# Kernel optimization log

Hardware: AMD Instinct MI355X
Metric: run time of the kernel (lower is better)

The kernel has to match this reference:

```python
import jax, jax.numpy as jnp
import numpy as np

D = 128        # feature_dims
ITERS = 2      # update_iters
B, R = 8, 256  # n segments (proteins), residues per segment
NEG_SLOPE = 0.1

def leaky(x):
    return jax.nn.leaky_relu(x, NEG_SLOPE)

def setup_inputs() -> dict:
    key = jax.random.key(0)
    ks = jax.random.split(key, 13)
    def w(k, shape):
        fan_in = shape[0]
        return jax.random.normal(k, shape, jnp.float32) / np.sqrt(fan_in)
    return {
        "fresidues": jax.random.normal(ks[0], (B, R, 20), jnp.float32),
        "coordinates": jax.random.normal(ks[1], (B, R, 3), jnp.float32) * 10.0,
        "W_emb": w(ks[2], (20, D)),                    # res_embedding (no bias)
        "W_e1": w(ks[3], (2 * D + 1, D)),              # linear_e layer 1
        "b_e1": jnp.zeros((D,), jnp.float32),
        "W_e2": w(ks[4], (D, D)),                      # linear_e layer 2
        "b_e2": jnp.zeros((D,), jnp.float32),
        "W_inf": w(ks[5], (D, 1)),                     # linear_inf gate
        "b_inf": jnp.zeros((1,), jnp.float32),
        "W_h1": w(ks[6], (2 * D, D)),                  # linear_h layer 1
        "b_h1": jnp.zeros((D,), jnp.float32),
        "W_h2": w(ks[7], (D, D)),                      # linear_h layer 2
        "b_h2": jnp.zeros((D,), jnp.float32),
    }

def reference(fresidues, coordinates, W_emb, W_e1, b_e1, W_e2, b_e2,
              W_inf, b_inf, W_h1, b_h1, W_h2, b_h2):
    # h: [B,R,D]
    h = leaky(fresidues @ W_emb)
    # pairwise squared distances: [B,R,R,1], constant across iterations
    d2 = jnp.sum(jnp.square(coordinates[:, :, None, :] - coordinates[:, None, :, :]),
                 axis=-1, keepdims=True)
    # mask out self-edges (1 - eye): [1,R,R,1]
    mask = (1.0 - jnp.eye(R, dtype=h.dtype))[None, :, :, None]
    # split edge-MLP first-layer weights to avoid materializing the [B,R,R,2D+1] concat:
    # m_input = cat([h_i, h_j, d2]) @ W_e1  ==  h_i@W_i + h_j@W_j + d2*w_d
    W_i, W_j, w_d = W_e1[:D], W_e1[D:2 * D], W_e1[2 * D]
    for _ in range(ITERS):
        ti = h @ W_i                                   # [B,R,D] receiver part
        tj = h @ W_j                                   # [B,R,D] sender part
        pre = ti[:, :, None, :] + tj[:, None, :, :] + d2 * w_d + b_e1  # [B,R,R,D]
        m = leaky(leaky(pre) @ W_e2 + b_e2)            # [B,R,R,D]
        e = jax.nn.sigmoid(m @ W_inf + b_inf) * mask   # [B,R,R,1]
        m_pre = jnp.sum(m * e, axis=2)                 # sum over senders j -> [B,R,D]
        hm = jnp.concatenate([h, m_pre], axis=-1)      # [B,R,2D]
        h = (leaky(hm @ W_h1 + b_h1) @ W_h2 + b_h2) + h
    return h

if __name__ == "__main__":
    out = reference(**setup_inputs())
    print(out.shape, out.dtype)
```

## Files before the change

kernel.cpp:

```cpp
#include <hip/hip_runtime.h>

typedef unsigned short ushort_t;
typedef __attribute__((ext_vector_type(8))) short shortx8;
typedef __attribute__((ext_vector_type(4))) float floatx4;
typedef __attribute__((ext_vector_type(2))) float floatx2;

#define NS 0.1f

__device__ __forceinline__ ushort_t f2bf_rne(float f) {
  union { float f; unsigned int u; } v; v.f = f;
  unsigned int r = v.u + 0x7FFFu + ((v.u >> 16) & 1u);
  return (ushort_t)(r >> 16);
}
__device__ __forceinline__ unsigned int pk2bf(float a, float b) {
  union { float f; unsigned int u; } x, y; x.f = a; y.f = b;
  return __builtin_amdgcn_perm(y.u + 0x8000u, x.u + 0x8000u, 0x07060302u);
}
__device__ __forceinline__ ushort_t f2bf_rhu(float f) {
  union { float f; unsigned int u; } v; v.f = f;
  return (ushort_t)((v.u + 0x8000u) >> 16);
}
__device__ __forceinline__ float lk(float x) { return fmaxf(x, NS * x); }
__device__ __forceinline__ floatx2 lk2(floatx2 v) {
  return __builtin_elementwise_max(v, v * (floatx2){NS, NS});
}

__global__ __launch_bounds__(256) void prep_w(
    const float* __restrict__ W_e1, const float* __restrict__ W_e2,
    const float* __restrict__ W_h1, const float* __restrict__ W_h2,
    ushort_t* __restrict__ wijf, ushort_t* __restrict__ we2f,
    ushort_t* __restrict__ wh1f, ushort_t* __restrict__ wh2f) {
  int e = blockIdx.x * 256 + threadIdx.x;
  int which, le;
  if (e < 32768) { which = 0; le = e; }
  else if (e < 49152) { which = 1; le = e - 32768; }
  else if (e < 81920) { which = 2; le = e - 49152; }
  else { which = 3; le = e - 81920; }
  const int NT = (which == 0) ? 16 : 8;
  int f = le >> 3, j = le & 7;
  int lane = f & 63, ft = f >> 6;
  int t = ft % NT, s = ft / NT;
  int n = t * 16 + (lane & 15), k = s * 32 + (lane >> 4) * 8 + j;
  float v; ushort_t* d;
  if (which == 0) { v = (n < 128) ? W_e1[k * 128 + n] : W_e1[(128 + k) * 128 + (n - 128)]; d = wijf; }
  else if (which == 1) { v = W_e2[k * 128 + n]; d = we2f; }
  else if (which == 2) { v = W_h1[k * 128 + n]; d = wh1f; }
  else { v = W_h2[k * 128 + n]; d = wh2f; }
  d[le] = f2bf_rne(v);
}

__device__ __forceinline__ void proj_store(float v, int m, int n,
                                           float* __restrict__ ti, float* __restrict__ tjf) {
  if (n < 128) {
    ti[(size_t)m * 128 + n] = v;
  } else {
    int k = n - 128, b = m >> 8, j = m & 255;
    int s = k >> 5, lg2 = (k >> 3) & 3, j8 = k & 7;
    tjf[((((size_t)(b * 4 + s)) * 256 + j) * 4 + lg2) * 8 + j8] = v;
  }
}

__global__ __launch_bounds__(256) void h0_proj(
    const float* __restrict__ fres, const float* __restrict__ Wemb,
    const ushort_t* __restrict__ wijf, float* __restrict__ h_out,
    float* __restrict__ ti, float* __restrict__ tjf) {
  const int m0 = blockIdx.x * 16;
  const int tid = threadIdx.x;
  const int w = tid >> 6, lane = tid & 63, l16 = lane & 15, lg = lane >> 4;
  __shared__ __align__(16) ushort_t sH[16][136];
  {
    const int row = tid >> 4, c0 = (tid & 15) * 8;
    const float* fr = fres + (size_t)(m0 + row) * 20;
    float a[8] = {0, 0, 0, 0, 0, 0, 0, 0};
    for (int k = 0; k < 20; ++k) {
      float fv = fr[k];
      float4 w0 = *(const float4*)(Wemb + k * 128 + c0);
      float4 w1 = *(const float4*)(Wemb + k * 128 + c0 + 4);
      a[0] += fv * w0.x; a[1] += fv * w0.y; a[2] += fv * w0.z; a[3] += fv * w0.w;
      a[4] += fv * w1.x; a[5] += fv * w1.y; a[6] += fv * w1.z; a[7] += fv * w1.w;
    }
#pragma unroll
    for (int x = 0; x < 8; ++x) a[x] = lk(a[x]);
    float* ho = h_out + (size_t)(m0 + row) * 128 + c0;
    *(float4*)ho = (float4){a[0], a[1], a[2], a[3]};
    *(float4*)(ho + 4) = (float4){a[4], a[5], a[6], a[7]};
    unsigned int* sh = (unsigned int*)&sH[row][c0];
    sh[0] = pk2bf(a[0], a[1]); sh[1] = pk2bf(a[2], a[3]);
    sh[2] = pk2bf(a[4], a[5]); sh[3] = pk2bf(a[6], a[7]);
  }
  __syncthreads();
  floatx4 ap[4];
#pragma unroll
  for (int q = 0; q < 4; ++q) ap[q] = (floatx4){0.f, 0.f, 0.f, 0.f};
  const shortx8* Wp = (const shortx8*)wijf;
#pragma unroll
  for (int s = 0; s < 4; ++s) {
    shortx8 af = *(const shortx8*)&sH[l16][s * 32 + lg * 8];
#pragma unroll
    for (int q = 0; q < 4; ++q)
      ap[q] = __builtin_amdgcn_mfma_f32_16x16x32_bf16(af, Wp[(s * 16 + 4 * w + q) * 64 + lane], ap[q], 0, 0, 0);
  }
#pragma unroll
  for (int q = 0; q < 4; ++q) {
    const int n = (4 * w + q) * 16 + l16;
#pragma unroll
    for (int r = 0; r < 4; ++r) proj_store(ap[q][r], m0 + lg * 4 + r, n, ti, tjf);
  }
}

__global__ __launch_bounds__(256, 3) void edge_kernel(
    const float* __restrict__ ti, const float* __restrict__ tjf,
    const float* __restrict__ coords, const ushort_t* __restrict__ we2f,
    const float* __restrict__ W_e1, const float* __restrict__ b_e1,
    const float* __restrict__ b_e2, const float* __restrict__ W_inf,
    const float* __restrict__ b_inf, float* __restrict__ mp0, float* __restrict__ mp1) {
  const int blk = blockIdx.x;
  const int b = blk >> 9, i = (blk >> 1) & 255, ch = blk & 1;
  const int tid = threadIdx.x;
  const int w = tid >> 6, lane = tid & 63, l16 = lane & 15, lg = lane >> 4;

  __shared__ __align__(16) ushort_t sW[16384];
  __shared__ __align__(16) float sTiP[128];
  __shared__ __align__(16) float sWd[128];
  __shared__ __align__(16) float sD2[128];
  __shared__ __align__(16) float sMp[4][128];

  {
    shortx8* dst = (shortx8*)sW;
    const shortx8* src = (const shortx8*)we2f;
#pragma unroll
    for (int r = 0; r < 8; ++r) dst[r * 256 + tid] = src[r * 256 + tid];
  }
  if (tid < 128) {
    sTiP[tid] = ti[(size_t)(b * 256 + i) * 128 + tid] + b_e1[tid];
    sWd[tid] = W_e1[256 * 128 + tid];
    const int j = ch * 128 + tid;
    float dx = coords[(size_t)(b * 256 + i) * 3 + 0] - coords[(size_t)(b * 256 + j) * 3 + 0];
    float dy = coords[(size_t)(b * 256 + i) * 3 + 1] - coords[(size_t)(b * 256 + j) * 3 + 1];
    float dz = coords[(size_t)(b * 256 + i) * 3 + 2] - coords[(size_t)(b * 256 + j) * 3 + 2];
    sD2[tid] = dx * dx + dy * dy + dz * dz;
  }
  floatx4 acc[2][8];
#pragma unroll
  for (int t = 0; t < 8; ++t) {
    float bv = b_e2[t * 16 + l16];
    acc[0][t] = (floatx4){bv, bv, bv, bv};
    acc[1][t] = acc[0][t];
  }
  __syncthreads();

  float d2a[2];
  d2a[0] = sD2[w * 16 + l16];
  d2a[1] = sD2[64 + w * 16 + l16];
  const shortx8* sWf = (const shortx8*)sW;

#pragma unroll
  for (int s = 0; s < 4; ++s) {
    const int k0 = s * 32 + lg * 8;
    floatx2 p2[4], w2[4];
#pragma unroll
    for (int x = 0; x < 4; ++x) {
      p2[x] = *(const floatx2*)&sTiP[k0 + 2 * x];
      w2[x] = *(const floatx2*)&sWd[k0 + 2 * x];
    }
    shortx8 af[2];
#pragma unroll
    for (int c = 0; c < 2; ++c) {
      const int jr = ch * 128 + c * 64 + w * 16 + l16;
      const float* tb = tjf + (((size_t)(b * 4 + s) * 256 + jr) * 4 + lg) * 8;
      float4 t0 = *(const float4*)tb;
      float4 t1 = *(const float4*)(tb + 4);
      const floatx2 d2v = (floatx2){d2a[c], d2a[c]};
      floatx2 pr0 = (floatx2){t0.x, t0.y} + (p2[0] + d2v * w2[0]);
      floatx2 pr1 = (floatx2){t0.z, t0.w} + (p2[1] + d2v * w2[1]);
      floatx2 pr2 = (floatx2){t1.x, t1.y} + (p2[2] + d2v * w2[2]);
      floatx2 pr3 = (floatx2){t1.z, t1.w} + (p2[3] + d2v * w2[3]);
      floatx2 l0 = lk2(pr0), l1 = lk2(pr1), l2 = lk2(pr2), l3 = lk2(pr3);
      union { shortx8 s8; unsigned int u[4]; } A;
      A.u[0] = pk2bf(l0.x, l0.y); A.u[1] = pk2bf(l1.x, l1.y);
      A.u[2] = pk2bf(l2.x, l2.y); A.u[3] = pk2bf(l3.x, l3.y);
      af[c] = A.s8;
    }
#pragma unroll
    for (int tg = 0; tg < 2; ++tg) {
      shortx8 b0 = sWf[(s * 8 + tg * 4 + 0) * 64 + lane];
      shortx8 b1 = sWf[(s * 8 + tg * 4 + 1) * 64 + lane];
      shortx8 b2 = sWf[(s * 8 + tg * 4 + 2) * 64 + lane];
      shortx8 b3 = sWf[(s * 8 + tg * 4 + 3) * 64 + lane];
#pragma unroll
      for (int c = 0; c < 2; ++c) {
        acc[c][tg * 4 + 0] = __builtin_amdgcn_mfma_f32_16x16x32_bf16(af[c], b0, acc[c][tg * 4 + 0], 0, 0, 0);
        acc[c][tg * 4 + 1] = __builtin_amdgcn_mfma_f32_16x16x32_bf16(af[c], b1, acc[c][tg * 4 + 1], 0, 0, 0);
        acc[c][tg * 4 + 2] = __builtin_amdgcn_mfma_f32_16x16x32_bf16(af[c], b2, acc[c][tg * 4 + 2], 0, 0, 0);
        acc[c][tg * 4 + 3] = __builtin_amdgcn_mfma_f32_16x16x32_bf16(af[c], b3, acc[c][tg * 4 + 3], 0, 0, 0);
      }
    }
  }

  float winfv[8], mp[8];
#pragma unroll
  for (int t = 0; t < 8; ++t) { winfv[t] = W_inf[t * 16 + l16]; mp[t] = 0.f; }
  const float binf = b_inf[0];
#pragma unroll
  for (int c = 0; c < 2; ++c) {
#pragma unroll
    for (int t = 0; t < 8; ++t) {
      floatx2 v0 = lk2((floatx2){acc[c][t][0], acc[c][t][1]});
      floatx2 v1 = lk2((floatx2){acc[c][t][2], acc[c][t][3]});
      acc[c][t][0] = v0.x; acc[c][t][1] = v0.y; acc[c][t][2] = v1.x; acc[c][t][3] = v1.y;
    }
    float p[4];
#pragma unroll
    for (int r = 0; r < 4; ++r) {
      float sum = 0.f;
#pragma unroll
      for (int t = 0; t < 8; ++t) sum += acc[c][t][r] * winfv[t];
      p[r] = sum;
    }
#pragma unroll
    for (int off = 1; off <= 8; off <<= 1)
#pragma unroll
      for (int r = 0; r < 4; ++r) p[r] += __shfl_xor(p[r], off);
#pragma unroll
    for (int r = 0; r < 4; ++r) {
      const int jg = ch * 128 + c * 64 + w * 16 + lg * 4 + r;
      float x = p[r] + binf;
      float e = __builtin_amdgcn_rcpf(1.f + __expf(-x));
      if (jg == i) e = 0.f;
#pragma unroll
      for (int t = 0; t < 8; ++t) mp[t] += acc[c][t][r] * e;
    }
  }
#pragma unroll
  for (int t = 0; t < 8; ++t) {
    mp[t] += __shfl_xor(mp[t], 16);
    mp[t] += __shfl_xor(mp[t], 32);
  }
  if (lg == 0) {
#pragma unroll
    for (int t = 0; t < 8; ++t) sMp[w][t * 16 + l16] = mp[t];
  }
  __syncthreads();
  if (tid < 128) {
    float v = sMp[0][tid] + sMp[1][tid] + sMp[2][tid] + sMp[3][tid];
    float* mpo = ch ? mp1 : mp0;
    mpo[(size_t)(b * 256 + i) * 128 + tid] = v;
  }
}

__global__ __launch_bounds__(256) void node_kernel(
    const float* __restrict__ h_in, const float* __restrict__ mp0, const float* __restrict__ mp1,
    const ushort_t* __restrict__ wh1f, const float* __restrict__ b_h1,
    const ushort_t* __restrict__ wh2f, const float* __restrict__ b_h2,
    const ushort_t* __restrict__ wijf, float* __restrict__ h_out,
    float* __restrict__ ti, float* __restrict__ tjf, const int do_proj) {
  const int m0 = blockIdx.x * 16;
  const int tid = threadIdx.x;
  const int w = tid >> 6, lane = tid & 63, l16 = lane & 15, lg = lane >> 4;
  __shared__ __align__(16) ushort_t sA[16][264];
  __shared__ __align__(16) ushort_t sU[16][136];
  __shared__ __align__(16) ushort_t sHp[16][136];

  {
    const int row = tid >> 4, c0 = (tid & 15) * 16;
    unsigned int* dst = (unsigned int*)&sA[row][c0];
    if (c0 < 128) {
      const float* src = h_in + (size_t)(m0 + row) * 128 + c0;
#pragma unroll
      for (int x = 0; x < 8; ++x) dst[x] = pk2bf(src[2 * x], src[2 * x + 1]);
    } else {
      const float* s0 = mp0 + (size_t)(m0 + row) * 128 + (c0 - 128);
      const float* s1 = mp1 + (size_t)(m0 + row) * 128 + (c0 - 128);
#pragma unroll
      for (int x = 0; x < 8; ++x)
        dst[x] = pk2bf(s0[2 * x] + s1[2 * x], s0[2 * x + 1] + s1[2 * x + 1]);
    }
  }
  __syncthreads();
  floatx4 au[2];
#pragma unroll
  for (int q = 0; q < 2; ++q) { float bv = b_h1[(2 * w + q) * 16 + l16]; au[q] = (floatx4){bv, bv, bv, bv}; }
  const shortx8* W1 = (const shortx8*)wh1f;
#pragma unroll
  for (int s = 0; s < 8; ++s) {
    shortx8 af = *(const shortx8*)&sA[l16][s * 32 + lg * 8];
#pragma unroll
    for (int q = 0; q < 2; ++q)
      au[q] = __builtin_amdgcn_mfma_f32_16x16x32_bf16(af, W1[(s * 8 + 2 * w + q) * 64 + lane], au[q], 0, 0, 0);
  }
#pragma unroll
  for (int q = 0; q < 2; ++q)
#pragma unroll
    for (int r = 0; r < 4; ++r)
      sU[lg * 4 + r][(2 * w + q) * 16 + l16] = f2bf_rhu(lk(au[q][r]));
  __syncthreads();
  floatx4 ah[2];
#pragma unroll
  for (int q = 0; q < 2; ++q) { float bv = b_h2[(2 * w + q) * 16 + l16]; ah[q] = (floatx4){bv, bv, bv, bv}; }
  const shortx8* W2 = (const shortx8*)wh2f;
#pragma unroll
  for (int s = 0; s < 4; ++s) {
    shortx8 af = *(const shortx8*)&sU[l16][s * 32 + lg * 8];
#pragma unroll
    for (int q = 0; q < 2; ++q)
      ah[q] = __builtin_amdgcn_mfma_f32_16x16x32_bf16(af, W2[(s * 8 + 2 * w + q) * 64 + lane], ah[q], 0, 0, 0);
  }
#pragma unroll
  for (int q = 0; q < 2; ++q) {
    const int n = (2 * w + q) * 16 + l16;
#pragma unroll
    for (int r = 0; r < 4; ++r) {
      const int m = m0 + lg * 4 + r;
      float v = ah[q][r] + h_in[(size_t)m * 128 + n];
      h_out[(size_t)m * 128 + n] = v;
      sHp[lg * 4 + r][n] = f2bf_rhu(v);
    }
  }
  if (!do_proj) return;
  __syncthreads();
  floatx4 ap[4];
#pragma unroll
  for (int q = 0; q < 4; ++q) ap[q] = (floatx4){0.f, 0.f, 0.f, 0.f};
  const shortx8* Wp = (const shortx8*)wijf;
#pragma unroll
  for (int s = 0; s < 4; ++s) {
    shortx8 af = *(const shortx8*)&sHp[l16][s * 32 + lg * 8];
#pragma unroll
    for (int q = 0; q < 4; ++q)
      ap[q] = __builtin_amdgcn_mfma_f32_16x16x32_bf16(af, Wp[(s * 16 + 4 * w + q) * 64 + lane], ap[q], 0, 0, 0);
  }
#pragma unroll
  for (int q = 0; q < 4; ++q) {
    const int n = (4 * w + q) * 16 + l16;
#pragma unroll
    for (int r = 0; r < 4; ++r) proj_store(ap[q][r], m0 + lg * 4 + r, n, ti, tjf);
  }
}

extern "C" void kernel_launch(void* const* d_in, const int* in_sizes, int n_in,
                              void* d_out, int out_size, void* d_ws, size_t ws_size,
                              hipStream_t stream) {
  const float* fres   = (const float*)d_in[0];
  const float* coords = (const float*)d_in[1];
  const float* W_emb  = (const float*)d_in[2];
  const float* W_e1   = (const float*)d_in[3];
  const float* b_e1   = (const float*)d_in[4];
  const float* W_e2   = (const float*)d_in[5];
  const float* b_e2   = (const float*)d_in[6];
  const float* W_inf  = (const float*)d_in[7];
  const float* b_inf  = (const float*)d_in[8];
  const float* W_h1   = (const float*)d_in[9];
  const float* b_h1   = (const float*)d_in[10];
  const float* W_h2   = (const float*)d_in[11];
  const float* b_h2   = (const float*)d_in[12];
  float* out = (float*)d_out;

  char* ws = (char*)d_ws;
  float* hA  = (float*)(ws + (0 << 20));
  float* hB  = (float*)(ws + (1 << 20));
  float* tib = (float*)(ws + (2 << 20));
  float* tjf = (float*)(ws + (3 << 20));
  float* mp0 = (float*)(ws + (4 << 20));
  float* mp1 = (float*)(ws + (5 << 20));
  ushort_t* wijf = (ushort_t*)(ws + (6 << 20));
  ushort_t* we2f = wijf + 32768;
  ushort_t* wh1f = we2f + 16384;
  ushort_t* wh2f = wh1f + 32768;

  prep_w<<<384, 256, 0, stream>>>(W_e1, W_e2, W_h1, W_h2, wijf, we2f, wh1f, wh2f);
  h0_proj<<<128, 256, 0, stream>>>(fres, W_emb, wijf, hA, tib, tjf);

  edge_kernel<<<4096, 256, 0, stream>>>(tib, tjf, coords, we2f, W_e1, b_e1, b_e2, W_inf, b_inf, mp0, mp1);
  node_kernel<<<128, 256, 0, stream>>>(hA, mp0, mp1, wh1f, b_h1, wh2f, b_h2, wijf, hB, tib, tjf, 1);

  edge_kernel<<<4096, 256, 0, stream>>>(tib, tjf, coords, we2f, W_e1, b_e1, b_e2, W_inf, b_inf, mp0, mp1);
  node_kernel<<<128, 256, 0, stream>>>(hB, mp0, mp1, wh1f, b_h1, wh2f, b_h2, wijf, out, tib, tjf, 0);
}
```

Measured before the change: 177.0 us.

## Process all senders per receiver in one 512-thread block, use hardware bf16 pack

Each edge block now covers all 256 senders for one receiver with 8 waves instead of splitting senders into two 128-wide halves. This halves how many times the W_e2 tile is staged into shared memory and removes the second partial message buffer and its add in the node kernel. The bf16 packing switches to the v_cvt_pk_bf16_f32 instruction, and MFMA sections are wrapped in s_setprio. The larger block may change occupancy and rounding behaviour.

```diff
diff --git a/kernel.cpp b/kernel.cpp
--- a/kernel.cpp
+++ b/kernel.cpp
@@ -15,6 +15,11 @@
 __device__ __forceinline__ unsigned int pk2bf(float a, float b) {
   union { float f; unsigned int u; } x, y; x.f = a; y.f = b;
   return __builtin_amdgcn_perm(y.u + 0x8000u, x.u + 0x8000u, 0x07060302u);
+}
+__device__ __forceinline__ unsigned int cvtpk_bf16(float a, float b) {
+  unsigned int r;
+  asm("v_cvt_pk_bf16_f32 %0, %1, %2" : "=v"(r) : "v"(a), "v"(b));
+  return r;
 }
 __device__ __forceinline__ ushort_t f2bf_rhu(float f) {
   union { float f; unsigned int u; } v; v.f = f;
@@ -108,37 +113,38 @@
   }
 }
 
-__global__ __launch_bounds__(256, 3) void edge_kernel(
+__global__ __launch_bounds__(512, 4) void edge_kernel(
     const float* __restrict__ ti, const float* __restrict__ tjf,
     const float* __restrict__ coords, const ushort_t* __restrict__ we2f,
     const float* __restrict__ W_e1, const float* __restrict__ b_e1,
     const float* __restrict__ b_e2, const float* __restrict__ W_inf,
-    const float* __restrict__ b_inf, float* __restrict__ mp0, float* __restrict__ mp1) {
+    const float* __restrict__ b_inf, float* __restrict__ mp) {
   const int blk = blockIdx.x;
-  const int b = blk >> 9, i = (blk >> 1) & 255, ch = blk & 1;
+  const int b = blk >> 8, i = blk & 255;
   const int tid = threadIdx.x;
   const int w = tid >> 6, lane = tid & 63, l16 = lane & 15, lg = lane >> 4;
 
   __shared__ __align__(16) ushort_t sW[16384];
   __shared__ __align__(16) float sTiP[128];
   __shared__ __align__(16) float sWd[128];
-  __shared__ __align__(16) float sD2[128];
-  __shared__ __align__(16) float sMp[4][128];
+  __shared__ __align__(16) float sD2[256];
+  __shared__ __align__(16) float sMp[8][128];
 
   {
     shortx8* dst = (shortx8*)sW;
     const shortx8* src = (const shortx8*)we2f;
 #pragma unroll
-    for (int r = 0; r < 8; ++r) dst[r * 256 + tid] = src[r * 256 + tid];
+    for (int r = 0; r < 4; ++r) dst[r * 512 + tid] = src[r * 512 + tid];
   }
   if (tid < 128) {
     sTiP[tid] = ti[(size_t)(b * 256 + i) * 128 + tid] + b_e1[tid];
     sWd[tid] = W_e1[256 * 128 + tid];
-    const int j = ch * 128 + tid;
+  } else if (tid >= 256) {
+    const int j = tid - 256;
     float dx = coords[(size_t)(b * 256 + i) * 3 + 0] - coords[(size_t)(b * 256 + j) * 3 + 0];
     float dy = coords[(size_t)(b * 256 + i) * 3 + 1] - coords[(size_t)(b * 256 + j) * 3 + 1];
     float dz = coords[(size_t)(b * 256 + i) * 3 + 2] - coords[(size_t)(b * 256 + j) * 3 + 2];
-    sD2[tid] = dx * dx + dy * dy + dz * dz;
+    sD2[j] = dx * dx + dy * dy + dz * dz;
   }
   floatx4 acc[2][8];
 #pragma unroll
@@ -151,7 +157,7 @@
 
   float d2a[2];
   d2a[0] = sD2[w * 16 + l16];
-  d2a[1] = sD2[64 + w * 16 + l16];
+  d2a[1] = sD2[128 + w * 16 + l16];
   const shortx8* sWf = (const shortx8*)sW;
 
 #pragma unroll
@@ -166,19 +172,18 @@
     shortx8 af[2];
 #pragma unroll
     for (int c = 0; c < 2; ++c) {
-      const int jr = ch * 128 + c * 64 + w * 16 + l16;
+      const int jr = c * 128 + w * 16 + l16;
       const float* tb = tjf + (((size_t)(b * 4 + s) * 256 + jr) * 4 + lg) * 8;
       float4 t0 = *(const float4*)tb;
       float4 t1 = *(const float4*)(tb + 4);
       const floatx2 d2v = (floatx2){d2a[c], d2a[c]};
-      floatx2 pr0 = (floatx2){t0.x, t0.y} + (p2[0] + d2v * w2[0]);
-      floatx2 pr1 = (floatx2){t0.z, t0.w} + (p2[1] + d2v * w2[1]);
-      floatx2 pr2 = (floatx2){t1.x, t1.y} + (p2[2] + d2v * w2[2]);
-      floatx2 pr3 = (floatx2){t1.z, t1.w} + (p2[3] + d2v * w2[3]);
-      floatx2 l0 = lk2(pr0), l1 = lk2(pr1), l2 = lk2(pr2), l3 = lk2(pr3);
+      floatx2 l0 = lk2((floatx2){t0.x, t0.y} + (p2[0] + d2v * w2[0]));
+      floatx2 l1 = lk2((floatx2){t0.z, t0.w} + (p2[1] + d2v * w2[1]));
+      floatx2 l2 = lk2((floatx2){t1.x, t1.y} + (p2[2] + d2v * w2[2]));
+      floatx2 l3 = lk2((floatx2){t1.z, t1.w} + (p2[3] + d2v * w2[3]));
       union { shortx8 s8; unsigned int u[4]; } A;
-      A.u[0] = pk2bf(l0.x, l0.y); A.u[1] = pk2bf(l1.x, l1.y);
-      A.u[2] = pk2bf(l2.x, l2.y); A.u[3] = pk2bf(l3.x, l3.y);
+      A.u[0] = cvtpk_bf16(l0.x, l0.y); A.u[1] = cvtpk_bf16(l1.x, l1.y);
+      A.u[2] = cvtpk_bf16(l2.x, l2.y); A.u[3] = cvtpk_bf16(l3.x, l3.y);
       af[c] = A.s8;
     }
 #pragma unroll
@@ -187,6 +192,7 @@
       shortx8 b1 = sWf[(s * 8 + tg * 4 + 1) * 64 + lane];
       shortx8 b2 = sWf[(s * 8 + tg * 4 + 2) * 64 + lane];
       shortx8 b3 = sWf[(s * 8 + tg * 4 + 3) * 64 + lane];
+      __builtin_amdgcn_s_setprio(1);
 #pragma unroll
       for (int c = 0; c < 2; ++c) {
         acc[c][tg * 4 + 0] = __builtin_amdgcn_mfma_f32_16x16x32_bf16(af[c], b0, acc[c][tg * 4 + 0], 0, 0, 0);
@@ -194,12 +200,13 @@
         acc[c][tg * 4 + 2] = __builtin_amdgcn_mfma_f32_16x16x32_bf16(af[c], b2, acc[c][tg * 4 + 2], 0, 0, 0);
         acc[c][tg * 4 + 3] = __builtin_amdgcn_mfma_f32_16x16x32_bf16(af[c], b3, acc[c][tg * 4 + 3], 0, 0, 0);
       }
-    }
-  }
-
-  float winfv[8], mp[8];
-#pragma unroll
-  for (int t = 0; t < 8; ++t) { winfv[t] = W_inf[t * 16 + l16]; mp[t] = 0.f; }
+      __builtin_amdgcn_s_setprio(0);
+    }
+  }
+
+  float winfv[8], mpacc[8];
+#pragma unroll
+  for (int t = 0; t < 8; ++t) { winfv[t] = W_inf[t * 16 + l16]; mpacc[t] = 0.f; }
   const float binf = b_inf[0];
 #pragma unroll
   for (int c = 0; c < 2; ++c) {
@@ -223,33 +230,33 @@
       for (int r = 0; r < 4; ++r) p[r] += __shfl_xor(p[r], off);
 #pragma unroll
     for (int r = 0; r < 4; ++r) {
-      const int jg = ch * 128 + c * 64 + w * 16 + lg * 4 + r;
+      const int jg = c * 128 + w * 16 + lg * 4 + r;
       float x = p[r] + binf;
       float e = __builtin_amdgcn_rcpf(1.f + __expf(-x));
       if (jg == i) e = 0.f;
 #pragma unroll
-      for (int t = 0; t < 8; ++t) mp[t] += acc[c][t][r] * e;
+      for (int t = 0; t < 8; ++t) mpacc[t] += acc[c][t][r] * e;
     }
   }
 #pragma unroll
   for (int t = 0; t < 8; ++t) {
-    mp[t] += __shfl_xor(mp[t], 16);
-    mp[t] += __shfl_xor(mp[t], 32);
+    mpacc[t] += __shfl_xor(mpacc[t], 16);
+    mpacc[t] += __shfl_xor(mpacc[t], 32);
   }
   if (lg == 0) {
 #pragma unroll
-    for (int t = 0; t < 8; ++t) sMp[w][t * 16 + l16] = mp[t];
+    for (int t = 0; t < 8; ++t) sMp[w][t * 16 + l16] = mpacc[t];
   }
   __syncthreads();
   if (tid < 128) {
-    float v = sMp[0][tid] + sMp[1][tid] + sMp[2][tid] + sMp[3][tid];
-    float* mpo = ch ? mp1 : mp0;
-    mpo[(size_t)(b * 256 + i) * 128 + tid] = v;
+    float v = sMp[0][tid] + sMp[1][tid] + sMp[2][tid] + sMp[3][tid]
+            + sMp[4][tid] + sMp[5][tid] + sMp[6][tid] + sMp[7][tid];
+    mp[(size_t)(b * 256 + i) * 128 + tid] = v;
   }
 }
 
 __global__ __launch_bounds__(256) void node_kernel(
-    const float* __restrict__ h_in, const float* __restrict__ mp0, const float* __restrict__ mp1,
+    const float* __restrict__ h_in, const float* __restrict__ mp,
     const ushort_t* __restrict__ wh1f, const float* __restrict__ b_h1,
     const ushort_t* __restrict__ wh2f, const float* __restrict__ b_h2,
     const ushort_t* __restrict__ wijf, float* __restrict__ h_out,
@@ -269,11 +276,9 @@
 #pragma unroll
       for (int x = 0; x < 8; ++x) dst[x] = pk2bf(src[2 * x], src[2 * x + 1]);
     } else {
-      const float* s0 = mp0 + (size_t)(m0 + row) * 128 + (c0 - 128);
-      const float* s1 = mp1 + (size_t)(m0 + row) * 128 + (c0 - 128);
-#pragma unroll
-      for (int x = 0; x < 8; ++x)
-        dst[x] = pk2bf(s0[2 * x] + s1[2 * x], s0[2 * x + 1] + s1[2 * x + 1]);
+      const float* s0 = mp + (size_t)(m0 + row) * 128 + (c0 - 128);
+#pragma unroll
+      for (int x = 0; x < 8; ++x) dst[x] = pk2bf(s0[2 * x], s0[2 * x + 1]);
     }
   }
   __syncthreads();
@@ -360,8 +365,7 @@
   float* hB  = (float*)(ws + (1 << 20));
   float* tib = (float*)(ws + (2 << 20));
   float* tjf = (float*)(ws + (3 << 20));
-  float* mp0 = (float*)(ws + (4 << 20));
-  float* mp1 = (float*)(ws + (5 << 20));
+  float* mpb = (float*)(ws + (4 << 20));
   ushort_t* wijf = (ushort_t*)(ws + (6 << 20));
   ushort_t* we2f = wijf + 32768;
   ushort_t* wh1f = we2f + 16384;
@@ -370,9 +374,9 @@
   prep_w<<<384, 256, 0, stream>>>(W_e1, W_e2, W_h1, W_h2, wijf, we2f, wh1f, wh2f);
   h0_proj<<<128, 256, 0, stream>>>(fres, W_emb, wijf, hA, tib, tjf);
 
-  edge_kernel<<<4096, 256, 0, stream>>>(tib, tjf, coords, we2f, W_e1, b_e1, b_e2, W_inf, b_inf, mp0, mp1);
-  node_kernel<<<128, 256, 0, stream>>>(hA, mp0, mp1, wh1f, b_h1, wh2f, b_h2, wijf, hB, tib, tjf, 1);
-
-  edge_kernel<<<4096, 256, 0, stream>>>(tib, tjf, coords, we2f, W_e1, b_e1, b_e2, W_inf, b_inf, mp0, mp1);
-  node_kernel<<<128, 256, 0, stream>>>(hB, mp0, mp1, wh1f, b_h1, wh2f, b_h2, wijf, out, tib, tjf, 0);
-}
+  edge_kernel<<<2048, 512, 0, stream>>>(tib, tjf, coords, we2f, W_e1, b_e1, b_e2, W_inf, b_inf, mpb);
+  node_kernel<<<128, 256, 0, stream>>>(hA, mpb, wh1f, b_h1, wh2f, b_h2, wijf, hB, tib, tjf, 1);
+
+  edge_kernel<<<2048, 512, 0, stream>>>(tib, tjf, coords, we2f, W_e1, b_e1, b_e2, W_inf, b_inf, mpb);
+  node_kernel<<<128, 256, 0, stream>>>(hB, mpb, wh1f, b_h1, wh2f, b_h2, wijf, out, tib, tjf, 0);
+}
```

Measured after the change: 180.9 us. 1.02x slower.

## Process two receivers per edge block to reuse W_e2 tile and sender loads

Applied to the files above, without the earlier changes.

Each edge_kernel block now handles two receiver residues instead of one, halving the grid. The per-block LDS load of W_e2, the tj global loads and the B-fragment LDS reads are amortized over twice the MFMA work. The change also swaps the manual bf16 packing for v_cvt_pk_bf16_f32, replaces shuffle-based row reductions with DPP adds, and raises MFMA issue priority with s_setprio. The cost is doubled accumulator registers, with launch bounds lowered from 3 to 2 blocks per CU, which may reduce occupancy.

```diff
diff --git a/kernel.cpp b/kernel.cpp
--- a/kernel.cpp
+++ b/kernel.cpp
@@ -16,6 +16,11 @@
   union { float f; unsigned int u; } x, y; x.f = a; y.f = b;
   return __builtin_amdgcn_perm(y.u + 0x8000u, x.u + 0x8000u, 0x07060302u);
 }
+__device__ __forceinline__ unsigned int cvtpk_bf16(float a, float b) {
+  unsigned int r;
+  asm("v_cvt_pk_bf16_f32 %0, %1, %2" : "=v"(r) : "v"(a), "v"(b));
+  return r;
+}
 __device__ __forceinline__ ushort_t f2bf_rhu(float f) {
   union { float f; unsigned int u; } v; v.f = f;
   return (ushort_t)((v.u + 0x8000u) >> 16);
@@ -23,6 +28,19 @@
 __device__ __forceinline__ float lk(float x) { return fmaxf(x, NS * x); }
 __device__ __forceinline__ floatx2 lk2(floatx2 v) {
   return __builtin_elementwise_max(v, v * (floatx2){NS, NS});
+}
+
+__device__ __forceinline__ float row16_sum(float x) {
+  int t;
+  t = __builtin_amdgcn_update_dpp(0, __builtin_bit_cast(int, x), 0x128, 0xF, 0xF, true);
+  x += __builtin_bit_cast(float, t);
+  t = __builtin_amdgcn_update_dpp(0, __builtin_bit_cast(int, x), 0x124, 0xF, 0xF, true);
+  x += __builtin_bit_cast(float, t);
+  t = __builtin_amdgcn_update_dpp(0, __builtin_bit_cast(int, x), 0x4E, 0xF, 0xF, true);
+  x += __builtin_bit_cast(float, t);
+  t = __builtin_amdgcn_update_dpp(0, __builtin_bit_cast(int, x), 0xB1, 0xF, 0xF, true);
+  x += __builtin_bit_cast(float, t);
+  return x;
 }
 
 __global__ __launch_bounds__(256) void prep_w(
@@ -108,22 +126,25 @@
   }
 }
 
-__global__ __launch_bounds__(256, 3) void edge_kernel(
+__global__ __launch_bounds__(256, 2) void edge_kernel(
     const float* __restrict__ ti, const float* __restrict__ tjf,
     const float* __restrict__ coords, const ushort_t* __restrict__ we2f,
     const float* __restrict__ W_e1, const float* __restrict__ b_e1,
     const float* __restrict__ b_e2, const float* __restrict__ W_inf,
     const float* __restrict__ b_inf, float* __restrict__ mp0, float* __restrict__ mp1) {
   const int blk = blockIdx.x;
-  const int b = blk >> 9, i = (blk >> 1) & 255, ch = blk & 1;
+  const int ch = blk & 1;
+  const int ip = (blk >> 1) & 127;
+  const int b = blk >> 8;
+  const int i0 = ip * 2;
   const int tid = threadIdx.x;
   const int w = tid >> 6, lane = tid & 63, l16 = lane & 15, lg = lane >> 4;
 
   __shared__ __align__(16) ushort_t sW[16384];
-  __shared__ __align__(16) float sTiP[128];
+  __shared__ __align__(16) float sTiP[2][128];
   __shared__ __align__(16) float sWd[128];
-  __shared__ __align__(16) float sD2[128];
-  __shared__ __align__(16) float sMp[4][128];
+  __shared__ __align__(16) float sD2[2][128];
+  __shared__ __align__(16) float sMp[2][4][128];
 
   {
     shortx8* dst = (shortx8*)sW;
@@ -132,54 +153,67 @@
     for (int r = 0; r < 8; ++r) dst[r * 256 + tid] = src[r * 256 + tid];
   }
   if (tid < 128) {
-    sTiP[tid] = ti[(size_t)(b * 256 + i) * 128 + tid] + b_e1[tid];
+    sTiP[0][tid] = ti[(size_t)(b * 256 + i0) * 128 + tid] + b_e1[tid];
     sWd[tid] = W_e1[256 * 128 + tid];
-    const int j = ch * 128 + tid;
-    float dx = coords[(size_t)(b * 256 + i) * 3 + 0] - coords[(size_t)(b * 256 + j) * 3 + 0];
-    float dy = coords[(size_t)(b * 256 + i) * 3 + 1] - coords[(size_t)(b * 256 + j) * 3 + 1];
-    float dz = coords[(size_t)(b * 256 + i) * 3 + 2] - coords[(size_t)(b * 256 + j) * 3 + 2];
-    sD2[tid] = dx * dx + dy * dy + dz * dz;
-  }
-  floatx4 acc[2][8];
+  } else {
+    const int t2 = tid - 128;
+    sTiP[1][t2] = ti[(size_t)(b * 256 + i0 + 1) * 128 + t2] + b_e1[t2];
+  }
+  {
+    const int ii = tid >> 7, jj = tid & 127;
+    const int iv = i0 + ii, jv = ch * 128 + jj;
+    float dx = coords[(size_t)(b * 256 + iv) * 3 + 0] - coords[(size_t)(b * 256 + jv) * 3 + 0];
+    float dy = coords[(size_t)(b * 256 + iv) * 3 + 1] - coords[(size_t)(b * 256 + jv) * 3 + 1];
+    float dz = coords[(size_t)(b * 256 + iv) * 3 + 2] - coords[(size_t)(b * 256 + jv) * 3 + 2];
+    sD2[ii][jj] = dx * dx + dy * dy + dz * dz;
+  }
+
+  floatx4 acc[2][2][8];
 #pragma unroll
   for (int t = 0; t < 8; ++t) {
     float bv = b_e2[t * 16 + l16];
-    acc[0][t] = (floatx4){bv, bv, bv, bv};
-    acc[1][t] = acc[0][t];
-  }
-  __syncthreads();
-
-  float d2a[2];
-  d2a[0] = sD2[w * 16 + l16];
-  d2a[1] = sD2[64 + w * 16 + l16];
+    floatx4 v = (floatx4){bv, bv, bv, bv};
+    acc[0][0][t] = v; acc[0][1][t] = v; acc[1][0][t] = v; acc[1][1][t] = v;
+  }
+  __syncthreads();
+
+  float d2a[2][2];
+#pragma unroll
+  for (int ii = 0; ii < 2; ++ii)
+#pragma unroll
+    for (int c = 0; c < 2; ++c)
+      d2a[ii][c] = sD2[ii][c * 64 + w * 16 + l16];
   const shortx8* sWf = (const shortx8*)sW;
 
 #pragma unroll
   for (int s = 0; s < 4; ++s) {
     const int k0 = s * 32 + lg * 8;
-    floatx2 p2[4], w2[4];
-#pragma unroll
-    for (int x = 0; x < 4; ++x) {
-      p2[x] = *(const floatx2*)&sTiP[k0 + 2 * x];
-      w2[x] = *(const floatx2*)&sWd[k0 + 2 * x];
-    }
-    shortx8 af[2];
+    floatx2 w2[4];
+#pragma unroll
+    for (int x = 0; x < 4; ++x) w2[x] = *(const floatx2*)&sWd[k0 + 2 * x];
+    shortx8 af[2][2];
 #pragma unroll
     for (int c = 0; c < 2; ++c) {
       const int jr = ch * 128 + c * 64 + w * 16 + l16;
       const float* tb = tjf + (((size_t)(b * 4 + s) * 256 + jr) * 4 + lg) * 8;
       float4 t0 = *(const float4*)tb;
       float4 t1 = *(const float4*)(tb + 4);
-      const floatx2 d2v = (floatx2){d2a[c], d2a[c]};
-      floatx2 pr0 = (floatx2){t0.x, t0.y} + (p2[0] + d2v * w2[0]);
-      floatx2 pr1 = (floatx2){t0.z, t0.w} + (p2[1] + d2v * w2[1]);
-      floatx2 pr2 = (floatx2){t1.x, t1.y} + (p2[2] + d2v * w2[2]);
-      floatx2 pr3 = (floatx2){t1.z, t1.w} + (p2[3] + d2v * w2[3]);
-      floatx2 l0 = lk2(pr0), l1 = lk2(pr1), l2 = lk2(pr2), l3 = lk2(pr3);
-      union { shortx8 s8; unsigned int u[4]; } A;
-      A.u[0] = pk2bf(l0.x, l0.y); A.u[1] = pk2bf(l1.x, l1.y);
-      A.u[2] = pk2bf(l2.x, l2.y); A.u[3] = pk2bf(l3.x, l3.y);
-      af[c] = A.s8;
+#pragma unroll
+      for (int ii = 0; ii < 2; ++ii) {
+        floatx2 p0 = *(const floatx2*)&sTiP[ii][k0 + 0];
+        floatx2 p1 = *(const floatx2*)&sTiP[ii][k0 + 2];
+        floatx2 p2v = *(const floatx2*)&sTiP[ii][k0 + 4];
+        floatx2 p3 = *(const floatx2*)&sTiP[ii][k0 + 6];
+        const floatx2 d2v = (floatx2){d2a[ii][c], d2a[ii][c]};
+        floatx2 l0 = lk2((floatx2){t0.x, t0.y} + (p0 + d2v * w2[0]));
+        floatx2 l1 = lk2((floatx2){t0.z, t0.w} + (p1 + d2v * w2[1]));
+        floatx2 l2 = lk2((floatx2){t1.x, t1.y} + (p2v + d2v * w2[2]));
+        floatx2 l3 = lk2((floatx2){t1.z, t1.w} + (p3 + d2v * w2[3]));
+        union { shortx8 s8; unsigned int u[4]; } A;
+        A.u[0] = cvtpk_bf16(l0.x, l0.y); A.u[1] = cvtpk_bf16(l1.x, l1.y);
+        A.u[2] = cvtpk_bf16(l2.x, l2.y); A.u[3] = cvtpk_bf16(l3.x, l3.y);
+        af[ii][c] = A.s8;
+      }
     }
 #pragma unroll
     for (int tg = 0; tg < 2; ++tg) {
@@ -187,64 +221,69 @@
       shortx8 b1 = sWf[(s * 8 + tg * 4 + 1) * 64 + lane];
       shortx8 b2 = sWf[(s * 8 + tg * 4 + 2) * 64 + lane];
       shortx8 b3 = sWf[(s * 8 + tg * 4 + 3) * 64 + lane];
-#pragma unroll
-      for (int c = 0; c < 2; ++c) {
-        acc[c][tg * 4 + 0] = __builtin_amdgcn_mfma_f32_16x16x32_bf16(af[c], b0, acc[c][tg * 4 + 0], 0, 0, 0);
-        acc[c][tg * 4 + 1] = __builtin_amdgcn_mfma_f32_16x16x32_bf16(af[c], b1, acc[c][tg * 4 + 1], 0, 0, 0);
-        acc[c][tg * 4 + 2] = __builtin_amdgcn_mfma_f32_16x16x32_bf16(af[c], b2, acc[c][tg * 4 + 2], 0, 0, 0);
-        acc[c][tg * 4 + 3] = __builtin_amdgcn_mfma_f32_16x16x32_bf16(af[c], b3, acc[c][tg * 4 + 3], 0, 0, 0);
+      __builtin_amdgcn_s_setprio(1);
+#pragma unroll
+      for (int ii = 0; ii < 2; ++ii)
+#pragma unroll
+        for (int c = 0; c < 2; ++c) {
+          acc[ii][c][tg * 4 + 0] = __builtin_amdgcn_mfma_f32_16x16x32_bf16(af[ii][c], b0, acc[ii][c][tg * 4 + 0], 0, 0, 0);
+          acc[ii][c][tg * 4 + 1] = __builtin_amdgcn_mfma_f32_16x16x32_bf16(af[ii][c], b1, acc[ii][c][tg * 4 + 1], 0, 0, 0);
+          acc[ii][c][tg * 4 + 2] = __builtin_amdgcn_mfma_f32_16x16x32_bf16(af[ii][c], b2, acc[ii][c][tg * 4 + 2], 0, 0, 0);
+          acc[ii][c][tg * 4 + 3] = __builtin_amdgcn_mfma_f32_16x16x32_bf16(af[ii][c], b3, acc[ii][c][tg * 4 + 3], 0, 0, 0);
+        }
+      __builtin_amdgcn_s_setprio(0);
+    }
+  }
+
+  float winfv[8];
+#pragma unroll
+  for (int t = 0; t < 8; ++t) winfv[t] = W_inf[t * 16 + l16];
+  const float binf = b_inf[0];
+#pragma unroll
+  for (int ii = 0; ii < 2; ++ii) {
+    const int i = i0 + ii;
+    float mpacc[8];
+#pragma unroll
+    for (int t = 0; t < 8; ++t) mpacc[t] = 0.f;
+#pragma unroll
+    for (int c = 0; c < 2; ++c) {
+#pragma unroll
+      for (int t = 0; t < 8; ++t) {
+        floatx2 v0 = lk2((floatx2){acc[ii][c][t][0], acc[ii][c][t][1]});
+        floatx2 v1 = lk2((floatx2){acc[ii][c][t][2], acc[ii][c][t][3]});
+        acc[ii][c][t][0] = v0.x; acc[ii][c][t][1] = v0.y;
+        acc[ii][c][t][2] = v1.x; acc[ii][c][t][3] = v1.y;
       }
-    }
-  }
-
-  float winfv[8], mp[8];
-#pragma unroll
-  for (int t = 0; t < 8; ++t) { winfv[t] = W_inf[t * 16 + l16]; mp[t] = 0.f; }
-  const float binf = b_inf[0];
-#pragma unroll
-  for (int c = 0; c < 2; ++c) {
+#pragma unroll
+      for (int r = 0; r < 4; ++r) {
+        float sum = 0.f;
+#pragma unroll
+        for (int t = 0; t < 8; ++t) sum += acc[ii][c][t][r] * winfv[t];
+        sum = row16_sum(sum);
+        const int jg = ch * 128 + c * 64 + w * 16 + lg * 4 + r;
+        float x = sum + binf;
+        float e = __builtin_amdgcn_rcpf(1.f + __expf(-x));
+        if (jg == i) e = 0.f;
+#pragma unroll
+        for (int t = 0; t < 8; ++t) mpacc[t] += acc[ii][c][t][r] * e;
+      }
+    }
 #pragma unroll
     for (int t = 0; t < 8; ++t) {
-      floatx2 v0 = lk2((floatx2){acc[c][t][0], acc[c][t][1]});
-      floatx2 v1 = lk2((floatx2){acc[c][t][2], acc[c][t][3]});
-      acc[c][t][0] = v0.x; acc[c][t][1] = v0.y; acc[c][t][2] = v1.x; acc[c][t][3] = v1.y;
-    }
-    float p[4];
-#pragma unroll
-    for (int r = 0; r < 4; ++r) {
-      float sum = 0.f;
-#pragma unroll
-      for (int t = 0; t < 8; ++t) sum += acc[c][t][r] * winfv[t];
-      p[r] = sum;
-    }
-#pragma unroll
-    for (int off = 1; off <= 8; off <<= 1)
-#pragma unroll
-      for (int r = 0; r < 4; ++r) p[r] += __shfl_xor(p[r], off);
-#pragma unroll
-    for (int r = 0; r < 4; ++r) {
-      const int jg = ch * 128 + c * 64 + w * 16 + lg * 4 + r;
-      float x = p[r] + binf;
-      float e = __builtin_amdgcn_rcpf(1.f + __expf(-x));
-      if (jg == i) e = 0.f;
-#pragma unroll
-      for (int t = 0; t < 8; ++t) mp[t] += acc[c][t][r] * e;
-    }
-  }
-#pragma unroll
-  for (int t = 0; t < 8; ++t) {
-    mp[t] += __shfl_xor(mp[t], 16);
-    mp[t] += __shfl_xor(mp[t], 32);
-  }
-  if (lg == 0) {
-#pragma unroll
-    for (int t = 0; t < 8; ++t) sMp[w][t * 16 + l16] = mp[t];
-  }
-  __syncthreads();
-  if (tid < 128) {
-    float v = sMp[0][tid] + sMp[1][tid] + sMp[2][tid] + sMp[3][tid];
+      mpacc[t] += __shfl_xor(mpacc[t], 16);
+      mpacc[t] += __shfl_xor(mpacc[t], 32);
+    }
+    if (lg == 0) {
+#pragma unroll
+      for (int t = 0; t < 8; ++t) sMp[ii][w][t * 16 + l16] = mpacc[t];
+    }
+  }
+  __syncthreads();
+  {
+    const int ii = tid >> 7, col = tid & 127;
+    float v = sMp[ii][0][col] + sMp[ii][1][col] + sMp[ii][2][col] + sMp[ii][3][col];
     float* mpo = ch ? mp1 : mp0;
-    mpo[(size_t)(b * 256 + i) * 128 + tid] = v;
+    mpo[(size_t)(b * 256 + i0 + ii) * 128 + col] = v;
   }
 }
 
@@ -370,9 +409,9 @@
   prep_w<<<384, 256, 0, stream>>>(W_e1, W_e2, W_h1, W_h2, wijf, we2f, wh1f, wh2f);
   h0_proj<<<128, 256, 0, stream>>>(fres, W_emb, wijf, hA, tib, tjf);
 
-  edge_kernel<<<4096, 256, 0, stream>>>(tib, tjf, coords, we2f, W_e1, b_e1, b_e2, W_inf, b_inf, mp0, mp1);
+  edge_kernel<<<2048, 256, 0, stream>>>(tib, tjf, coords, we2f, W_e1, b_e1, b_e2, W_inf, b_inf, mp0, mp1);
   node_kernel<<<128, 256, 0, stream>>>(hA, mp0, mp1, wh1f, b_h1, wh2f, b_h2, wijf, hB, tib, tjf, 1);
 
-  edge_kernel<<<4096, 256, 0, stream>>>(tib, tjf, coords, we2f, W_e1, b_e1, b_e2, W_inf, b_inf, mp0, mp1);
+  edge_kernel<<<2048, 256, 0, stream>>>(tib, tjf, coords, we2f, W_e1, b_e1, b_e2, W_inf, b_inf, mp0, mp1);
   node_kernel<<<128, 256, 0, stream>>>(hB, mp0, mp1, wh1f, b_h1, wh2f, b_h2, wijf, out, tib, tjf, 0);
 }
```

Measured after the change: 164.5 us. 7.1% less time.
